# Kernel optimization log

Hardware: AMD Instinct MI355X
Metric: run time of the kernel (lower is better)

## Reference

```python
import jax, jax.numpy as jnp
import numpy as np

EMBED_DIM = 768
NUM_HEADS = 12
HEAD_SIZE = EMBED_DIM // NUM_HEADS


def setup_inputs() -> dict:
    key = jax.random.key(0)
    ks = jax.random.split(key, 9)
    B, S, D = 4, 2048, EMBED_DIM
    scale = 1.0 / np.sqrt(D)
    x = jax.random.normal(ks[0], (B, S, D), dtype=jnp.float32)
    # Linear params (torch nn.Linear: y = x @ W.T + b); store W as [in, out] for einsum
    Wq = jax.random.normal(ks[1], (D, D), dtype=jnp.float32) * scale
    bq = jnp.zeros((D,), dtype=jnp.float32)
    Wk = jax.random.normal(ks[2], (D, D), dtype=jnp.float32) * scale
    bk = jnp.zeros((D,), dtype=jnp.float32)
    Wv = jax.random.normal(ks[3], (D, D), dtype=jnp.float32) * scale
    bv = jnp.zeros((D,), dtype=jnp.float32)
    Wo = jax.random.normal(ks[4], (D, D), dtype=jnp.float32) * scale
    bo = jnp.zeros((D,), dtype=jnp.float32)
    return {"x": x, "Wq": Wq, "bq": bq, "Wk": Wk, "bk": bk,
            "Wv": Wv, "bv": bv, "Wo": Wo, "bo": bo}


def reference(x, Wq, bq, Wk, bk, Wv, bv, Wo, bo):
    B, S, D = x.shape
    H, hs = NUM_HEADS, HEAD_SIZE
    scale = hs ** (-0.5)
    # Projections
    Q = (x @ Wq + bq).reshape(B, S, H, hs)
    K = (x @ Wk + bk).reshape(B, S, H, hs)
    V = (x @ Wv + bv).reshape(B, S, H, hs)
    # Batched attention over all heads (equivalent to the per-head loop:
    # torch view splits last dim into H contiguous chunks; concat of per-head
    # outputs along -1 restores the same layout)
    scores = jnp.einsum('bqhd,bkhd->bhqk', Q, K) * scale  # [B,H,S,S]
    attn = jax.nn.softmax(scores, axis=-1)
    out = jnp.einsum('bhqk,bkhd->bqhd', attn, V).reshape(B, S, D)
    # Output projection; dropout is identity in eval mode
    return out @ Wo + bo
```

## Files before the change

### kernel.cpp

```cpp
#include <hip/hip_runtime.h>

typedef unsigned short ushort_t;
typedef __bf16 bf16x8 __attribute__((ext_vector_type(8)));
typedef float floatx4 __attribute__((ext_vector_type(4)));

__device__ inline ushort_t f2bf(float f) {
    __bf16 h = (__bf16)f;
    return __builtin_bit_cast(ushort_t, h);
}

__device__ inline void gload16(const void* g, void* l) {
    __builtin_amdgcn_global_load_lds((const __attribute__((address_space(1))) void*)g,
                                     (__attribute__((address_space(3))) void*)l, 16, 0, 0);
}

__global__ __launch_bounds__(256) void prep_kernel(
    const float* __restrict__ x, ushort_t* __restrict__ xbf,
    const float* __restrict__ W0, const float* __restrict__ W1,
    const float* __restrict__ W2, const float* __restrict__ W3,
    ushort_t* __restrict__ T0, ushort_t* __restrict__ T1,
    ushort_t* __restrict__ T2, ushort_t* __restrict__ T3) {
    int bx = blockIdx.x;
    int tid = threadIdx.x;
    if (bx < 2304) {
        __shared__ float t[32][33];
        int w = bx / 576, rem = bx % 576;
        const float* W; ushort_t* T;
        switch (w) {
            case 0: W = W0; T = T0; break;
            case 1: W = W1; T = T1; break;
            case 2: W = W2; T = T2; break;
            default: W = W3; T = T3; break;
        }
        int n0 = (rem / 24) * 32, k0 = (rem % 24) * 32;
        int tx = tid & 31, ty = tid >> 5;
        for (int i = 0; i < 4; ++i)
            t[ty + i * 8][tx] = W[(k0 + ty + i * 8) * 768 + n0 + tx];
        __syncthreads();
        for (int i = 0; i < 4; ++i)
            T[(n0 + ty + i * 8) * 768 + k0 + tx] = f2bf(t[tx][ty + i * 8]);
    } else {
        int i = ((bx - 2304) * 256 + tid) * 4;
        float4 v = *(const float4*)(x + i);
        ushort4 u;
        u.x = f2bf(v.x); u.y = f2bf(v.y); u.z = f2bf(v.z); u.w = f2bf(v.w);
        *(ushort4*)(xbf + i) = u;
    }
}

__global__ __launch_bounds__(256) void gemm_qkv(
    const ushort_t* __restrict__ A,
    const ushort_t* __restrict__ Tq, const ushort_t* __restrict__ Tk, const ushort_t* __restrict__ Tv,
    const float* __restrict__ bq, const float* __restrict__ bk, const float* __restrict__ bv,
    ushort_t* __restrict__ Qb, ushort_t* __restrict__ Kb, ushort_t* __restrict__ Vtb) {
    __shared__ ushort_t As[128 * 64];
    __shared__ ushort_t Bs[128 * 64];
    int tid = threadIdx.x;
    int m0 = blockIdx.x * 128;
    int by = blockIdx.y;
    int which = by / 6;
    int n0 = (by % 6) * 128;
    const ushort_t* Bt = which == 0 ? Tq : (which == 1 ? Tk : Tv);
    const float* bias = which == 0 ? bq : (which == 1 ? bk : bv);

    int wave = tid >> 6;
    int lane = tid & 63;
    int ln = tid & 15;
    int quad = (tid >> 4) & 3;
    int wr = (wave >> 1) * 64;
    int wc = (wave & 1) * 64;
    int lr = lane >> 3;
    int lc = (lane & 7) * 8;

    floatx4 acc[4][4];
    floatx4 z = {0.f, 0.f, 0.f, 0.f};
    for (int i = 0; i < 4; ++i)
        for (int j = 0; j < 4; ++j) acc[i][j] = z;

    for (int kt = 0; kt < 12; ++kt) {
        int k0 = kt * 64;
        __syncthreads();
        for (int i = 0; i < 4; ++i) {
            int c = wave * 4 + i;
            gload16(&A[(m0 + c * 8 + lr) * 768 + k0 + lc], &As[c * 512]);
            gload16(&Bt[(n0 + c * 8 + lr) * 768 + k0 + lc], &Bs[c * 512]);
        }
        __syncthreads();
        for (int ks = 0; ks < 2; ++ks) {
            bf16x8 a[4], b[4];
            for (int i = 0; i < 4; ++i)
                a[i] = *(const bf16x8*)&As[(wr + i * 16 + ln) * 64 + ks * 32 + quad * 8];
            for (int j = 0; j < 4; ++j)
                b[j] = *(const bf16x8*)&Bs[(wc + j * 16 + ln) * 64 + ks * 32 + quad * 8];
            __builtin_amdgcn_s_setprio(1);
            for (int i = 0; i < 4; ++i)
                for (int j = 0; j < 4; ++j)
                    acc[i][j] = __builtin_amdgcn_mfma_f32_16x16x32_bf16(a[i], b[j], acc[i][j], 0, 0, 0);
            __builtin_amdgcn_s_setprio(0);
        }
    }

    const float QSCALE = 0.125f * 1.44269504088896f;
    for (int i = 0; i < 4; ++i) {
        for (int j = 0; j < 4; ++j) {
            int gn = n0 + wc + j * 16 + ln;
            float bia = bias[gn];
            int h = gn >> 6, dd = gn & 63;
            for (int r = 0; r < 4; ++r) {
                int gm = m0 + wr + i * 16 + quad * 4 + r;
                int bb = gm >> 11, ss = gm & 2047;
                float v = acc[i][j][r] + bia;
                if (which == 0) {
                    Qb[((bb * 12 + h) * 2048 + ss) * 64 + dd] = f2bf(v * QSCALE);
                } else if (which == 1) {
                    Kb[((bb * 12 + h) * 2048 + ss) * 64 + dd] = f2bf(v);
                } else {
                    Vtb[((bb * 12 + h) * 64 + dd) * 2048 + ss] = f2bf(v);
                }
            }
        }
    }
}

__global__ __launch_bounds__(256) void attn_kernel(
    const ushort_t* __restrict__ Qb, const ushort_t* __restrict__ Kb,
    const ushort_t* __restrict__ Vtb, ushort_t* __restrict__ Ob) {
    __shared__ ushort_t Ks[2][64 * 72];
    __shared__ ushort_t Vs[2][64 * 72];
    int tid = threadIdx.x;
    int qt = blockIdx.x;
    int bh = blockIdx.y;
    int wave = tid >> 6;
    int ln = tid & 15;
    int quad = (tid >> 4) & 3;
    int q0 = qt * 128 + wave * 32;

    const ushort_t* Qp = Qb + (size_t)bh * 2048 * 64;
    const ushort_t* Kp = Kb + (size_t)bh * 2048 * 64;
    const ushort_t* Vp = Vtb + (size_t)bh * 64 * 2048;

    bf16x8 bqf[2][2];
    for (int g = 0; g < 2; ++g)
        for (int ks = 0; ks < 2; ++ks)
            bqf[g][ks] = *(const bf16x8*)&Qp[(q0 + g * 16 + ln) * 64 + ks * 32 + quad * 8];

    int srow = tid >> 3;
    int c8 = tid & 7;
    int scol = c8 * 8;
    int u = c8 & 3;
    int vcol = (c8 >> 2) * 32 + (u & 1) * 16 + (u >> 1) * 4;

    uint4 kreg[2], vreg[2];

    for (int p = 0; p < 2; ++p) {
        kreg[p] = *(const uint4*)&Kp[(p * 32 + srow) * 64 + scol];
        vreg[p] = *(const uint4*)&Vp[(p * 32 + srow) * 2048 + scol];
    }
    for (int p = 0; p < 2; ++p) {
        *(uint4*)&Ks[0][(p * 32 + srow) * 72 + scol] = kreg[p];
        ushort_t* vb = &Vs[0][(p * 32 + srow) * 72 + vcol];
        *(uint2*)vb = make_uint2(vreg[p].x, vreg[p].y);
        *(uint2*)(vb + 8) = make_uint2(vreg[p].z, vreg[p].w);
    }
    __syncthreads();

    floatx4 o_acc[2][4];
    float lsum[2] = {0.f, 0.f};
    floatx4 z = {0.f, 0.f, 0.f, 0.f};
    for (int g = 0; g < 2; ++g)
        for (int m4 = 0; m4 < 4; ++m4) o_acc[g][m4] = z;

    for (int kt = 0; kt < 32; ++kt) {
        int cur = kt & 1;
        if (kt < 31) {
            for (int p = 0; p < 2; ++p) {
                kreg[p] = *(const uint4*)&Kp[((kt + 1) * 64 + p * 32 + srow) * 64 + scol];
                vreg[p] = *(const uint4*)&Vp[(p * 32 + srow) * 2048 + (kt + 1) * 64 + scol];
            }
        }

        const ushort_t* KsH = Ks[cur];
        const ushort_t* VsH = Vs[cur];

        bf16x8 ak[4][2];
        for (int m4 = 0; m4 < 4; ++m4)
            for (int ks = 0; ks < 2; ++ks)
                ak[m4][ks] = *(const bf16x8*)&KsH[(m4 * 16 + ln) * 72 + ks * 32 + quad * 8];

        floatx4 st[2][4];
        __builtin_amdgcn_s_setprio(1);
        for (int g = 0; g < 2; ++g)
            for (int m4 = 0; m4 < 4; ++m4) {
                floatx4 s = z;
                s = __builtin_amdgcn_mfma_f32_16x16x32_bf16(ak[m4][0], bqf[g][0], s, 0, 0, 0);
                s = __builtin_amdgcn_mfma_f32_16x16x32_bf16(ak[m4][1], bqf[g][1], s, 0, 0, 0);
                st[g][m4] = s;
            }
        __builtin_amdgcn_s_setprio(0);

        float pv[2][4][4];
        for (int g = 0; g < 2; ++g)
            for (int m4 = 0; m4 < 4; ++m4)
                for (int r = 0; r < 4; ++r) {
                    float e = __builtin_amdgcn_exp2f(st[g][m4][r]);
                    pv[g][m4][r] = e;
                    lsum[g] += e;
                }

        bf16x8 av[4][2];
        for (int m4 = 0; m4 < 4; ++m4)
            for (int c = 0; c < 2; ++c)
                av[m4][c] = *(const bf16x8*)&VsH[(m4 * 16 + ln) * 72 + c * 32 + quad * 8];

        for (int g = 0; g < 2; ++g) {
            bf16x8 bp[2];
            for (int c = 0; c < 2; ++c) {
                bf16x8 b;
                b[0] = (__bf16)pv[g][2 * c][0];
                b[1] = (__bf16)pv[g][2 * c][1];
                b[2] = (__bf16)pv[g][2 * c][2];
                b[3] = (__bf16)pv[g][2 * c][3];
                b[4] = (__bf16)pv[g][2 * c + 1][0];
                b[5] = (__bf16)pv[g][2 * c + 1][1];
                b[6] = (__bf16)pv[g][2 * c + 1][2];
                b[7] = (__bf16)pv[g][2 * c + 1][3];
                bp[c] = b;
            }
            __builtin_amdgcn_s_setprio(1);
            for (int m4 = 0; m4 < 4; ++m4)
                for (int c = 0; c < 2; ++c)
                    o_acc[g][m4] = __builtin_amdgcn_mfma_f32_16x16x32_bf16(av[m4][c], bp[c], o_acc[g][m4], 0, 0, 0);
            __builtin_amdgcn_s_setprio(0);
        }

        if (kt < 31) {
            int nxt = cur ^ 1;
            for (int p = 0; p < 2; ++p) {
                *(uint4*)&Ks[nxt][(p * 32 + srow) * 72 + scol] = kreg[p];
                ushort_t* vb = &Vs[nxt][(p * 32 + srow) * 72 + vcol];
                *(uint2*)vb = make_uint2(vreg[p].x, vreg[p].y);
                *(uint2*)(vb + 8) = make_uint2(vreg[p].z, vreg[p].w);
            }
        }
        __syncthreads();
    }

    for (int g = 0; g < 2; ++g) {
        lsum[g] += __shfl_xor(lsum[g], 16);
        lsum[g] += __shfl_xor(lsum[g], 32);
    }

    int b = bh / 12, h = bh % 12;
    for (int g = 0; g < 2; ++g) {
        float inv = 1.f / lsum[g];
        int token = b * 2048 + q0 + g * 16 + ln;
        for (int m4 = 0; m4 < 4; ++m4)
            for (int r = 0; r < 4; ++r)
                Ob[token * 768 + h * 64 + m4 * 16 + quad * 4 + r] = f2bf(o_acc[g][m4][r] * inv);
    }
}

__global__ __launch_bounds__(256) void gemm_out(
    const ushort_t* __restrict__ A, const ushort_t* __restrict__ Bt,
    const float* __restrict__ bias, float* __restrict__ out) {
    __shared__ ushort_t As[128 * 64];
    __shared__ ushort_t Bs[128 * 64];
    int tid = threadIdx.x;
    int m0 = blockIdx.x * 128;
    int n0 = blockIdx.y * 128;

    int wave = tid >> 6;
    int lane = tid & 63;
    int ln = tid & 15;
    int quad = (tid >> 4) & 3;
    int wr = (wave >> 1) * 64;
    int wc = (wave & 1) * 64;
    int lr = lane >> 3;
    int lc = (lane & 7) * 8;

    floatx4 acc[4][4];
    floatx4 z = {0.f, 0.f, 0.f, 0.f};
    for (int i = 0; i < 4; ++i)
        for (int j = 0; j < 4; ++j) acc[i][j] = z;

    for (int kt = 0; kt < 12; ++kt) {
        int k0 = kt * 64;
        __syncthreads();
        for (int i = 0; i < 4; ++i) {
            int c = wave * 4 + i;
            gload16(&A[(m0 + c * 8 + lr) * 768 + k0 + lc], &As[c * 512]);
            gload16(&Bt[(n0 + c * 8 + lr) * 768 + k0 + lc], &Bs[c * 512]);
        }
        __syncthreads();
        for (int ks = 0; ks < 2; ++ks) {
            bf16x8 a[4], b[4];
            for (int i = 0; i < 4; ++i)
                a[i] = *(const bf16x8*)&As[(wr + i * 16 + ln) * 64 + ks * 32 + quad * 8];
            for (int j = 0; j < 4; ++j)
                b[j] = *(const bf16x8*)&Bs[(wc + j * 16 + ln) * 64 + ks * 32 + quad * 8];
            __builtin_amdgcn_s_setprio(1);
            for (int i = 0; i < 4; ++i)
                for (int j = 0; j < 4; ++j)
                    acc[i][j] = __builtin_amdgcn_mfma_f32_16x16x32_bf16(a[i], b[j], acc[i][j], 0, 0, 0);
            __builtin_amdgcn_s_setprio(0);
        }
    }

    for (int i = 0; i < 4; ++i) {
        for (int j = 0; j < 4; ++j) {
            int gn = n0 + wc + j * 16 + ln;
            float bia = bias[gn];
            for (int r = 0; r < 4; ++r) {
                int gm = m0 + wr + i * 16 + quad * 4 + r;
                out[gm * 768 + gn] = acc[i][j][r] + bia;
            }
        }
    }
}

extern "C" void kernel_launch(void* const* d_in, const int* in_sizes, int n_in,
                              void* d_out, int out_size, void* d_ws, size_t ws_size,
                              hipStream_t stream) {
    const float* x  = (const float*)d_in[0];
    const float* Wq = (const float*)d_in[1];
    const float* bq = (const float*)d_in[2];
    const float* Wk = (const float*)d_in[3];
    const float* bk = (const float*)d_in[4];
    const float* Wv = (const float*)d_in[5];
    const float* bv = (const float*)d_in[6];
    const float* Wo = (const float*)d_in[7];
    const float* bo = (const float*)d_in[8];

    const int NTOK = 4 * 2048;
    const int NELT = NTOK * 768;
    const int WELT = 768 * 768;

    ushort_t* xbf = (ushort_t*)d_ws;
    ushort_t* Tq  = xbf + NELT;
    ushort_t* Tk  = Tq + WELT;
    ushort_t* Tv  = Tk + WELT;
    ushort_t* To  = Tv + WELT;
    ushort_t* Qb  = To + WELT;
    ushort_t* Kb  = Qb + NELT;
    ushort_t* Vtb = Kb + NELT;
    ushort_t* Ob  = Vtb + NELT;

    prep_kernel<<<8448, 256, 0, stream>>>(x, xbf, Wq, Wk, Wv, Wo, Tq, Tk, Tv, To);
    gemm_qkv<<<dim3(64, 18), 256, 0, stream>>>(xbf, Tq, Tk, Tv, bq, bk, bv, Qb, Kb, Vtb);
    attn_kernel<<<dim3(16, 48), 256, 0, stream>>>(Qb, Kb, Vtb, Ob);
    gemm_out<<<dim3(64, 6), 256, 0, stream>>>(Ob, To, bo, (float*)d_out);
}
```

Measured before the change: 255.0 us.

## Load attention K/V fragments directly from global memory, pre-permuting V layout

The attention kernel stops staging K and V tiles through double-buffered shared memory and instead has each wave load its MFMA fragments straight from global memory, which removes all block-level barriers in the key loop. To keep the V fragment loads contiguous, the QKV projection now writes the transposed V with a permuted sequence order inside each 64-key block. This matches the register packing of the P fragment that the LDS scatter used to produce. Each wave now issues redundant global/L2 reads of the same K/V tile that were shared before, and the loads are no longer prefetched a step ahead. The s_setprio hints around the MFMA loops are also removed in all kernels.

```diff
diff --git a/kernel.cpp b/kernel.cpp
--- a/kernel.cpp
+++ b/kernel.cpp
@@ -92,11 +92,9 @@
                 a[i] = *(const bf16x8*)&As[(wr + i * 16 + ln) * 64 + ks * 32 + quad * 8];
             for (int j = 0; j < 4; ++j)
                 b[j] = *(const bf16x8*)&Bs[(wc + j * 16 + ln) * 64 + ks * 32 + quad * 8];
-            __builtin_amdgcn_s_setprio(1);
             for (int i = 0; i < 4; ++i)
                 for (int j = 0; j < 4; ++j)
                     acc[i][j] = __builtin_amdgcn_mfma_f32_16x16x32_bf16(a[i], b[j], acc[i][j], 0, 0, 0);
-            __builtin_amdgcn_s_setprio(0);
         }
     }
 
@@ -115,7 +113,9 @@
                 } else if (which == 1) {
                     Kb[((bb * 12 + h) * 2048 + ss) * 64 + dd] = f2bf(v);
                 } else {
-                    Vtb[((bb * 12 + h) * 64 + dd) * 2048 + ss] = f2bf(v);
+                    int w = ss & 63;
+                    int mk = (w & 32) | ((w & 12) << 1) | ((w & 16) >> 2) | (w & 3);
+                    Vtb[((bb * 12 + h) * 64 + dd) * 2048 + (ss & ~63) + mk] = f2bf(v);
                 }
             }
         }
@@ -125,8 +125,6 @@
 __global__ __launch_bounds__(256) void attn_kernel(
     const ushort_t* __restrict__ Qb, const ushort_t* __restrict__ Kb,
     const ushort_t* __restrict__ Vtb, ushort_t* __restrict__ Ob) {
-    __shared__ ushort_t Ks[2][64 * 72];
-    __shared__ ushort_t Vs[2][64 * 72];
     int tid = threadIdx.x;
     int qt = blockIdx.x;
     int bh = blockIdx.y;
@@ -144,26 +142,6 @@
         for (int ks = 0; ks < 2; ++ks)
             bqf[g][ks] = *(const bf16x8*)&Qp[(q0 + g * 16 + ln) * 64 + ks * 32 + quad * 8];
 
-    int srow = tid >> 3;
-    int c8 = tid & 7;
-    int scol = c8 * 8;
-    int u = c8 & 3;
-    int vcol = (c8 >> 2) * 32 + (u & 1) * 16 + (u >> 1) * 4;
-
-    uint4 kreg[2], vreg[2];
-
-    for (int p = 0; p < 2; ++p) {
-        kreg[p] = *(const uint4*)&Kp[(p * 32 + srow) * 64 + scol];
-        vreg[p] = *(const uint4*)&Vp[(p * 32 + srow) * 2048 + scol];
-    }
-    for (int p = 0; p < 2; ++p) {
-        *(uint4*)&Ks[0][(p * 32 + srow) * 72 + scol] = kreg[p];
-        ushort_t* vb = &Vs[0][(p * 32 + srow) * 72 + vcol];
-        *(uint2*)vb = make_uint2(vreg[p].x, vreg[p].y);
-        *(uint2*)(vb + 8) = make_uint2(vreg[p].z, vreg[p].w);
-    }
-    __syncthreads();
-
     floatx4 o_acc[2][4];
     float lsum[2] = {0.f, 0.f};
     floatx4 z = {0.f, 0.f, 0.f, 0.f};
@@ -171,24 +149,17 @@
         for (int m4 = 0; m4 < 4; ++m4) o_acc[g][m4] = z;
 
     for (int kt = 0; kt < 32; ++kt) {
-        int cur = kt & 1;
-        if (kt < 31) {
-            for (int p = 0; p < 2; ++p) {
-                kreg[p] = *(const uint4*)&Kp[((kt + 1) * 64 + p * 32 + srow) * 64 + scol];
-                vreg[p] = *(const uint4*)&Vp[(p * 32 + srow) * 2048 + (kt + 1) * 64 + scol];
-            }
-        }
-
-        const ushort_t* KsH = Ks[cur];
-        const ushort_t* VsH = Vs[cur];
-
         bf16x8 ak[4][2];
         for (int m4 = 0; m4 < 4; ++m4)
             for (int ks = 0; ks < 2; ++ks)
-                ak[m4][ks] = *(const bf16x8*)&KsH[(m4 * 16 + ln) * 72 + ks * 32 + quad * 8];
+                ak[m4][ks] = *(const bf16x8*)&Kp[(kt * 64 + m4 * 16 + ln) * 64 + ks * 32 + quad * 8];
+
+        bf16x8 av[4][2];
+        for (int m4 = 0; m4 < 4; ++m4)
+            for (int c = 0; c < 2; ++c)
+                av[m4][c] = *(const bf16x8*)&Vp[(m4 * 16 + ln) * 2048 + kt * 64 + c * 32 + quad * 8];
 
         floatx4 st[2][4];
-        __builtin_amdgcn_s_setprio(1);
         for (int g = 0; g < 2; ++g)
             for (int m4 = 0; m4 < 4; ++m4) {
                 floatx4 s = z;
@@ -196,7 +167,6 @@
                 s = __builtin_amdgcn_mfma_f32_16x16x32_bf16(ak[m4][1], bqf[g][1], s, 0, 0, 0);
                 st[g][m4] = s;
             }
-        __builtin_amdgcn_s_setprio(0);
 
         float pv[2][4][4];
         for (int g = 0; g < 2; ++g)
@@ -206,11 +176,6 @@
                     pv[g][m4][r] = e;
                     lsum[g] += e;
                 }
-
-        bf16x8 av[4][2];
-        for (int m4 = 0; m4 < 4; ++m4)
-            for (int c = 0; c < 2; ++c)
-                av[m4][c] = *(const bf16x8*)&VsH[(m4 * 16 + ln) * 72 + c * 32 + quad * 8];
 
         for (int g = 0; g < 2; ++g) {
             bf16x8 bp[2];
@@ -226,23 +191,10 @@
                 b[7] = (__bf16)pv[g][2 * c + 1][3];
                 bp[c] = b;
             }
-            __builtin_amdgcn_s_setprio(1);
             for (int m4 = 0; m4 < 4; ++m4)
                 for (int c = 0; c < 2; ++c)
                     o_acc[g][m4] = __builtin_amdgcn_mfma_f32_16x16x32_bf16(av[m4][c], bp[c], o_acc[g][m4], 0, 0, 0);
-            __builtin_amdgcn_s_setprio(0);
-        }
-
-        if (kt < 31) {
-            int nxt = cur ^ 1;
-            for (int p = 0; p < 2; ++p) {
-                *(uint4*)&Ks[nxt][(p * 32 + srow) * 72 + scol] = kreg[p];
-                ushort_t* vb = &Vs[nxt][(p * 32 + srow) * 72 + vcol];
-                *(uint2*)vb = make_uint2(vreg[p].x, vreg[p].y);
-                *(uint2*)(vb + 8) = make_uint2(vreg[p].z, vreg[p].w);
-            }
-        }
-        __syncthreads();
+        }
     }
 
     for (int g = 0; g < 2; ++g) {
@@ -298,11 +250,9 @@
                 a[i] = *(const bf16x8*)&As[(wr + i * 16 + ln) * 64 + ks * 32 + quad * 8];
             for (int j = 0; j < 4; ++j)
                 b[j] = *(const bf16x8*)&Bs[(wc + j * 16 + ln) * 64 + ks * 32 + quad * 8];
-            __builtin_amdgcn_s_setprio(1);
             for (int i = 0; i < 4; ++i)
                 for (int j = 0; j < 4; ++j)
                     acc[i][j] = __builtin_amdgcn_mfma_f32_16x16x32_bf16(a[i], b[j], acc[i][j], 0, 0, 0);
-            __builtin_amdgcn_s_setprio(0);
         }
     }
 
```

Result: slower. 364.1 us (+42.8%).
